# Kernel tuning notes

Measured on AMD Instinct MI355X. Metric: run time of the kernel, lower is better.

Reference implementation:

```python
import jax, jax.numpy as jnp
import numpy as np
import math

N_HEAD = 16
HEAD_DIM = 32  # n_state // n_head // 2
THETA = 10000.0
LAMBDA_INIT = 0.8 - 0.6 * math.exp(-0.3 * 12)  # depth=12
EPS = 1e-5


def _rope_tables(seq_len):
    inv = 1.0 / (THETA ** (np.arange(0, HEAD_DIM, 2, dtype=np.float32) / HEAD_DIM))  # [hd/2]
    t = np.arange(seq_len, dtype=np.float32)
    freqs = np.outer(t, inv)  # [S, hd/2]
    return jnp.asarray(np.cos(freqs)), jnp.asarray(np.sin(freqs))


def _apply_rope_interleaved(x, cos, sin):
    # x: [B,S,H,D]; cos/sin: [S,D/2]; interleaved pairs (even, odd)
    x1, x2 = x[..., 0::2], x[..., 1::2]
    c = cos[None, :, None, :]
    s = sin[None, :, None, :]
    ye = x1 * c - x2 * s
    yo = x1 * s + x2 * c
    return jnp.stack([ye, yo], axis=-1).reshape(x.shape)


def setup_inputs() -> dict:
    key = jax.random.key(0)
    ks = jax.random.split(key, 10)
    B, S, D = 1, 2048, 1024
    hd = HEAD_DIM
    inp = {
        "x": jax.random.normal(ks[0], (B, S, D), jnp.float32),
        "Wq": jax.random.normal(ks[1], (D, D), jnp.float32) * 0.02,
        "Wk": jax.random.normal(ks[2], (D, D), jnp.float32) * 0.02,
        "Wv": jax.random.normal(ks[3], (D, D), jnp.float32) * 0.02,
        "Wo": jax.random.normal(ks[4], (D, D), jnp.float32) * 0.02,
        "lambda_q1": jax.random.normal(ks[5], (hd,), jnp.float32) * 0.1,
        "lambda_k1": jax.random.normal(ks[6], (hd,), jnp.float32) * 0.1,
        "lambda_q2": jax.random.normal(ks[7], (hd,), jnp.float32) * 0.1,
        "lambda_k2": jax.random.normal(ks[8], (hd,), jnp.float32) * 0.1,
        "gamma": jnp.ones((2 * hd,), jnp.float32),
    }
    return inp


def reference(x, Wq, Wk, Wv, Wo, lambda_q1, lambda_k1, lambda_q2, lambda_k2, gamma):
    B, S, D = x.shape
    H, hd = N_HEAD, HEAD_DIM

    q = x @ Wq.T
    k = x @ Wk.T
    v = x @ Wv.T

    q = q.reshape(B, S, 2 * H, hd)
    k = k.reshape(B, S, 2 * H, hd)
    v = v.reshape(B, S, H, 2, hd)

    cos, sin = _rope_tables(S)
    q = _apply_rope_interleaved(q, cos, sin)
    k = _apply_rope_interleaved(k, cos, sin)

    q = q.reshape(B, S, H, 2, hd)
    k = k.reshape(B, S, H, 2, hd)
    q1, q2 = q[:, :, :, 0], q[:, :, :, 1]
    k1, k2 = k[:, :, :, 0], k[:, :, :, 1]
    v1, v2 = v[:, :, :, 0], v[:, :, :, 1]

    scale = hd ** -0.5
    causal = jnp.tril(jnp.ones((S, S), dtype=bool))
    neg = jnp.finfo(x.dtype).min

    def probs(qh, kh):
        s = jnp.einsum('bihd,bjhd->bhij', qh, kh) * scale
        s = jnp.where(causal[None, None], s, neg)
        return jax.nn.softmax(s, axis=-1)

    p1 = probs(q1, k1)  # reused for v1 and v2 (attn11, attn12)
    a11 = jnp.einsum('bhij,bjhd->bihd', p1, v1)
    a12 = jnp.einsum('bhij,bjhd->bihd', p1, v2)
    attn1 = jnp.concatenate([a11, a12], axis=-1)  # [B,S,H,2hd]

    p2 = probs(q2, k2)
    a21 = jnp.einsum('bhij,bjhd->bihd', p2, v1)
    a22 = jnp.einsum('bhij,bjhd->bihd', p2, v2)
    attn2 = jnp.concatenate([a21, a22], axis=-1)

    lam1 = jnp.exp(jnp.sum(lambda_q1 * lambda_k1))
    lam2 = jnp.exp(jnp.sum(lambda_q2 * lambda_k2))
    lam = lam1 - lam2 + LAMBDA_INIT

    wv = attn1 - lam * attn2
    # RMSNorm over last dim (2*hd) with affine gamma
    wv = wv * jax.lax.rsqrt(jnp.mean(wv * wv, axis=-1, keepdims=True) + EPS) * gamma
    wv = wv * (1.0 - LAMBDA_INIT)

    wv = wv.reshape(B, S, H * 2 * hd)
    return wv @ Wo.T
```

## Files before the change

### kernel.cpp

```cpp
#include <hip/hip_runtime.h>
#include <hip/hip_bf16.h>
#include <math.h>


typedef __bf16 bf16x8 __attribute__((ext_vector_type(8)));
typedef float f32x4 __attribute__((ext_vector_type(4)));
typedef float f32x16 __attribute__((ext_vector_type(16)));

#define LOG2E 1.4426950408889634f
#define SCALE 0.17677669529663687f
#define C1EXP 0.25506100319239545f
#define DMAX_THR 31.36f
#define LAM_INIT 0.783605766532f
#define ONE_M_LI 0.216394233468f

#define GLOAD16(g, l)                                                              \
  __builtin_amdgcn_global_load_lds((const __attribute__((address_space(1))) void*)(g), \
                                   (__attribute__((address_space(3))) void*)(l), 16, 0, 0)

__device__ __forceinline__ ushort f2b(float f) {
  unsigned u = __builtin_bit_cast(unsigned, f);
  u += 0x7fffu + ((u >> 16) & 1u);
  return (ushort)(u >> 16);
}
__device__ __forceinline__ float b2f(ushort h) {
  return __builtin_bit_cast(float, ((unsigned)h) << 16);
}
__device__ __forceinline__ ushort f2h(float f) {
  _Float16 h = (_Float16)f;
  return __builtin_bit_cast(ushort, h);
}
__device__ __forceinline__ float h2f(ushort u) {
  return (float)__builtin_bit_cast(_Float16, u);
}
__device__ __forceinline__ int swz128(int row, int byteoff) {
  return row * 128 + (byteoff ^ ((row & 7) << 4));
}
__device__ __forceinline__ int qoff4(int qt) {
  int G = qt >> 2, rem = qt & 3;
  return 2 * G * (G + 1) + rem * (G + 1);
}
__device__ __forceinline__ f32x16 zero16() {
  f32x16 z;
#pragma unroll
  for (int i = 0; i < 16; ++i) z[i] = 0.f;
  return z;
}

__global__ __launch_bounds__(256) void prep_kernel(
    const float* __restrict__ x, const float* __restrict__ Wq,
    const float* __restrict__ Wk, const float* __restrict__ Wv,
    const float* __restrict__ Wo,
    ushort* __restrict__ xb, ushort* __restrict__ w1, ushort* __restrict__ wob,
    float* __restrict__ cosT, float* __restrict__ sinT) {
  unsigned b = blockIdx.x;
  if (b < 3072u) {
    unsigned i8 = (b * 256u + threadIdx.x) * 8u;
    const float* s;
    ushort* d;
    if (i8 < 2097152u) { s = x + i8; d = xb + i8; }
    else if (i8 < 3145728u) { s = Wq + (i8 - 2097152u); d = w1 + (i8 - 2097152u); }
    else if (i8 < 4194304u) { s = Wk + (i8 - 3145728u); d = w1 + (i8 - 2097152u); }
    else if (i8 < 5242880u) { s = Wv + (i8 - 4194304u); d = w1 + (i8 - 2097152u); }
    else { s = Wo + (i8 - 5242880u); d = wob + (i8 - 5242880u); }
    float4 v0 = *(const float4*)s;
    float4 v1 = *(const float4*)(s + 4);
    union { ushort h[8]; uint4 u; } o;
    o.h[0] = f2b(v0.x); o.h[1] = f2b(v0.y); o.h[2] = f2b(v0.z); o.h[3] = f2b(v0.w);
    o.h[4] = f2b(v1.x); o.h[5] = f2b(v1.y); o.h[6] = f2b(v1.z); o.h[7] = f2b(v1.w);
    *(uint4*)d = o.u;
    return;
  }
  unsigned j = (b - 3072u) * 256u + threadIdx.x;
  int tt = (int)(j >> 4), jj = (int)(j & 15u);
  float inv = powf(10000.0f, -(float)(2 * jj) * (1.0f / 32.0f));
  float ang = (float)tt * inv;
  cosT[j] = cosf(ang);
  sinT[j] = sinf(ang);
}

__global__ __launch_bounds__(256) void ropetv_kernel(ushort* __restrict__ qkv,
                                                     const float* __restrict__ cosT,
                                                     const float* __restrict__ sinT,
                                                     ushort* __restrict__ vt) {
  __shared__ __align__(16) ushort tile[64][80];
  const int t = threadIdx.x;
  if (blockIdx.x < 2048u) {
    unsigned i = blockIdx.x * 256u + t;
    int row = (int)(i >> 8), u4 = (int)(i & 255u);
    int colbase = (u4 < 128) ? (u4 * 8) : (1024 + (u4 - 128) * 8);
    int pbase = u4 * 4;
    ushort* p = qkv + (size_t)row * 3072 + colbase;
    uint4 v = *(const uint4*)p;
    unsigned vv[4] = {v.x, v.y, v.z, v.w};
    unsigned ov[4];
#pragma unroll
    for (int tpp = 0; tpp < 4; ++tpp) {
      int j = (pbase + tpp) & 15;
      float c = cosT[row * 16 + j], s = sinT[row * 16 + j];
      float x1 = b2f((ushort)(vv[tpp] & 0xffffu));
      float x2 = b2f((ushort)(vv[tpp] >> 16));
      float ye = x1 * c - x2 * s;
      float yo = x1 * s + x2 * c;
      ov[tpp] = (unsigned)f2b(ye) | ((unsigned)f2b(yo) << 16);
    }
    uint4 o = {ov[0], ov[1], ov[2], ov[3]};
    *(uint4*)p = o;
    return;
  }
  const int bb = (int)blockIdx.x - 2048;
  const int d0 = (bb & 15) * 64, s0 = (bb >> 4) * 64;
#pragma unroll
  for (int p = 0; p < 2; ++p) {
    int sl = p * 32 + (t >> 3), d8 = (t & 7) * 8;
    uint4 v = *(const uint4*)(qkv + (size_t)(s0 + sl) * 3072 + 2048 + d0 + d8);
    *(uint4*)(&tile[sl][d8]) = v;
  }
  __syncthreads();
#pragma unroll
  for (int p = 0; p < 2; ++p) {
    int dl = p * 32 + (t >> 3), s8 = (t & 7) * 8;
    union { ushort h[8]; uint4 u; } tmp;
#pragma unroll
    for (int jj = 0; jj < 8; ++jj) tmp.h[jj] = tile[s8 + jj][dl];
    *(uint4*)(vt + (size_t)(d0 + dl) * 2048 + s0 + s8) = tmp.u;
  }
}

template <int BM, int BN>
__global__ __launch_bounds__(256) void gemm_bt(const ushort* __restrict__ A,
                                               const ushort* __restrict__ B,
                                               void* __restrict__ C, int M, int N, int K,
                                               int out_bf16) {
  __shared__ __align__(16) ushort As[BM * 32];
  __shared__ __align__(16) ushort Bs[BN * 32];
  const int t = threadIdx.x, lane = t & 63, w = t >> 6;
  const int g = lane >> 4, r = lane & 15;
  const int wr = w >> 1, wc = w & 1;
  const int m0 = blockIdx.y * BM, n0 = blockIdx.x * BN;
  constexpr int AM = BM / 32, AN = BN / 32;

  f32x4 acc[AM][AN];
#pragma unroll
  for (int i = 0; i < AM; ++i)
#pragma unroll
    for (int j = 0; j < AN; ++j) acc[i][j] = (f32x4){0.f, 0.f, 0.f, 0.f};

  for (int k0 = 0; k0 < K; k0 += 32) {
    __syncthreads();
#pragma unroll
    for (int p = 0; p < BM / 64; ++p) {
      int idx = p * 256 + t;
      int row = idx >> 2, ko = (idx & 3) * 8;
      GLOAD16(A + (size_t)(m0 + row) * K + k0 + ko, As + idx * 8);
    }
#pragma unroll
    for (int p = 0; p < BN / 64; ++p) {
      int idx = p * 256 + t;
      int row = idx >> 2, ko = (idx & 3) * 8;
      GLOAD16(B + (size_t)(n0 + row) * K + k0 + ko, Bs + idx * 8);
    }
    __syncthreads();
    bf16x8 af[AM], bfr[AN];
#pragma unroll
    for (int i = 0; i < AM; ++i)
      af[i] = __builtin_bit_cast(bf16x8, *(const uint4*)(As + (wr * (BM / 2) + i * 16 + r) * 32 + g * 8));
#pragma unroll
    for (int i = 0; i < AN; ++i)
      bfr[i] = __builtin_bit_cast(bf16x8, *(const uint4*)(Bs + (wc * (BN / 2) + i * 16 + r) * 32 + g * 8));
#pragma unroll
    for (int mi = 0; mi < AM; ++mi)
#pragma unroll
      for (int ni = 0; ni < AN; ++ni)
        acc[mi][ni] = __builtin_amdgcn_mfma_f32_16x16x32_bf16(af[mi], bfr[ni], acc[mi][ni], 0, 0, 0);
  }
#pragma unroll
  for (int mi = 0; mi < AM; ++mi)
#pragma unroll
    for (int ni = 0; ni < AN; ++ni)
#pragma unroll
      for (int e = 0; e < 4; ++e) {
        int row = m0 + wr * (BM / 2) + mi * 16 + g * 4 + e;
        int col = n0 + wc * (BN / 2) + ni * 16 + r;
        float v = acc[mi][ni][e];
        if (out_bf16) ((ushort*)C)[(size_t)row * N + col] = f2b(v);
        else ((float*)C)[(size_t)row * N + col] = v;
      }
}

__global__ __launch_bounds__(256, 3) void attn_split_kernel(
    const ushort* __restrict__ qkv, const ushort* __restrict__ vt,
    ushort* __restrict__ pOh, float* __restrict__ pML) {
  __shared__ __align__(16) ushort Ks[64 * 64];
  __shared__ __align__(16) ushort Vs[64 * 64];

  int wi = blockIdx.x, qt = 0, c = 0;
  for (int q = 0; q < 32; ++q) {
    int nc = (q >> 2) + 1;
    if (wi < nc) { qt = q; c = wi; break; }
    wi -= nc;
  }
  const int h = blockIdx.y;
  const int pid = h * 144 + qoff4(qt) + c;
  const int t = threadIdx.x, lane = t & 63, w = t >> 6;
  const int sub = w & 1, qh = w >> 1;
  const int ql = lane & 31, g1 = lane >> 5;
  const int qa = qt * 64 + qh * 32 + ql;

  bf16x8 qf0 = __builtin_bit_cast(bf16x8, *(const uint4*)(qkv + (size_t)qa * 3072 + h * 64 + sub * 32 + g1 * 8));
  bf16x8 qf1 = __builtin_bit_cast(bf16x8, *(const uint4*)(qkv + (size_t)qa * 3072 + h * 64 + sub * 32 + 16 + g1 * 8));

  f32x16 O0 = zero16(), O1 = zero16();
  float mm = -1e30f, lsum = 0.f;

  const int ktb = c * 4;
  const int kte = min(ktb + 4, qt + 1);
  for (int kt = ktb; kt < kte; ++kt) {
    __syncthreads();
#pragma unroll
    for (int p = 0; p < 2; ++p) {
      int idx = (p * 4 + w) * 64 + lane;
      int row = idx >> 3;
      int kbs = ((idx & 7) * 16) ^ ((row & 7) << 4);
      const ushort* gk = qkv + (size_t)(kt * 64 + row) * 3072 + 1024 + h * 64 + (kbs >> 1);
      const ushort* gv = vt + (size_t)(h * 64 + row) * 2048 + kt * 64 + (kbs >> 1);
      GLOAD16(gk, Ks + (p * 4 + w) * 512);
      GLOAD16(gv, Vs + (p * 4 + w) * 512);
    }
    __syncthreads();

    f32x16 s0 = zero16(), s1 = zero16();
    {
      const int cb0 = (sub * 32 + g1 * 8) * 2;
      bf16x8 ka = __builtin_bit_cast(bf16x8, *(const uint4*)((const char*)Ks + swz128(ql, cb0)));
      bf16x8 kb = __builtin_bit_cast(bf16x8, *(const uint4*)((const char*)Ks + swz128(32 + ql, cb0)));
      const int cb1 = (sub * 32 + 16 + g1 * 8) * 2;
      bf16x8 kc = __builtin_bit_cast(bf16x8, *(const uint4*)((const char*)Ks + swz128(ql, cb1)));
      bf16x8 kd = __builtin_bit_cast(bf16x8, *(const uint4*)((const char*)Ks + swz128(32 + ql, cb1)));
      __builtin_amdgcn_s_setprio(1);
      s0 = __builtin_amdgcn_mfma_f32_32x32x16_bf16(ka, qf0, s0, 0, 0, 0);
      s1 = __builtin_amdgcn_mfma_f32_32x32x16_bf16(kb, qf0, s1, 0, 0, 0);
      s0 = __builtin_amdgcn_mfma_f32_32x32x16_bf16(kc, qf1, s0, 0, 0, 0);
      s1 = __builtin_amdgcn_mfma_f32_32x32x16_bf16(kd, qf1, s1, 0, 0, 0);
      __builtin_amdgcn_s_setprio(0);
    }

    if (kt == qt) {
      const int lim = qh * 32 + ql;
#pragma unroll
      for (int rg = 0; rg < 16; ++rg) {
        int kv0 = (rg & 3) + 4 * g1 + 8 * (rg >> 2);
        if (kv0 > lim) s0[rg] = -1e30f;
        if (kv0 + 32 > lim) s1[rg] = -1e30f;
      }
    }

    float rm = fmaxf(s0[0], s1[0]);
#pragma unroll
    for (int rg = 1; rg < 16; ++rg) rm = fmaxf(rm, fmaxf(s0[rg], s1[rg]));
    rm = fmaxf(rm, __shfl_xor(rm, 32));

    if (!__all(rm - mm <= DMAX_THR)) {
      float mn = fmaxf(mm, rm);
      float es = exp2f((mm - mn) * C1EXP);
      mm = mn;
      lsum *= es;
      O0 *= es;
      O1 *= es;
    }
    const float mnC = mm * C1EXP;
    float ps = 0.f;
#pragma unroll
    for (int rg = 0; rg < 16; ++rg) {
      float p0 = exp2f(__builtin_fmaf(s0[rg], C1EXP, -mnC));
      float p1 = exp2f(__builtin_fmaf(s1[rg], C1EXP, -mnC));
      s0[rg] = p0; s1[rg] = p1;
      ps += p0 + p1;
    }
    ps += __shfl_xor(ps, 32);
    lsum += ps;

    unsigned pk[2][4][2];
#pragma unroll
    for (int q2 = 0; q2 < 4; ++q2) {
      float a0 = s0[4 * q2 + 0], a1 = s0[4 * q2 + 1], a2 = s0[4 * q2 + 2], a3 = s0[4 * q2 + 3];
      float b0 = s1[4 * q2 + 0], b1 = s1[4 * q2 + 1], b2 = s1[4 * q2 + 2], b3 = s1[4 * q2 + 3];
      asm("v_cvt_pk_bf16_f32 %0, %1, %2" : "=v"(pk[0][q2][0]) : "v"(a0), "v"(a1));
      asm("v_cvt_pk_bf16_f32 %0, %1, %2" : "=v"(pk[0][q2][1]) : "v"(a2), "v"(a3));
      asm("v_cvt_pk_bf16_f32 %0, %1, %2" : "=v"(pk[1][q2][0]) : "v"(b0), "v"(b1));
      asm("v_cvt_pk_bf16_f32 %0, %1, %2" : "=v"(pk[1][q2][1]) : "v"(b2), "v"(b3));
    }
#pragma unroll
    for (int kvb = 0; kvb < 2; ++kvb) {
      asm volatile("v_permlane32_swap_b32 %0, %1" : "+v"(pk[kvb][0][0]), "+v"(pk[kvb][1][0]));
      asm volatile("v_permlane32_swap_b32 %0, %1" : "+v"(pk[kvb][0][1]), "+v"(pk[kvb][1][1]));
      asm volatile("v_permlane32_swap_b32 %0, %1" : "+v"(pk[kvb][2][0]), "+v"(pk[kvb][3][0]));
      asm volatile("v_permlane32_swap_b32 %0, %1" : "+v"(pk[kvb][2][1]), "+v"(pk[kvb][3][1]));
    }

#pragma unroll
    for (int ks = 0; ks < 4; ++ks) {
      const int kvb = ks >> 1, kshi = ks & 1;
      uint4 pu;
      pu.x = pk[kvb][2 * kshi][0];
      pu.y = pk[kvb][2 * kshi][1];
      pu.z = pk[kvb][2 * kshi + 1][0];
      pu.w = pk[kvb][2 * kshi + 1][1];
      bf16x8 pf = __builtin_bit_cast(bf16x8, pu);
      const int cb = (ks * 16 + g1 * 8) * 2;
      bf16x8 v0 = __builtin_bit_cast(bf16x8, *(const uint4*)((const char*)Vs + swz128(ql, cb)));
      bf16x8 v1 = __builtin_bit_cast(bf16x8, *(const uint4*)((const char*)Vs + swz128(32 + ql, cb)));
      __builtin_amdgcn_s_setprio(1);
      O0 = __builtin_amdgcn_mfma_f32_32x32x16_bf16(v0, pf, O0, 0, 0, 0);
      O1 = __builtin_amdgcn_mfma_f32_32x32x16_bf16(v1, pf, O1, 0, 0, 0);
      __builtin_amdgcn_s_setprio(0);
    }
  }

  const int qrow = qh * 32 + ql;
  float* pml = pML + (size_t)pid * 256 + sub * 128;
  if (g1 == 0) {
    pml[qrow] = mm;
    pml[64 + qrow] = lsum;
  }
  ushort* po = pOh + ((size_t)(pid * 2 + sub) * 64 + qrow) * 64;
#pragma unroll
  for (int q2 = 0; q2 < 4; ++q2) {
    uint2 u0, u1;
    u0.x = (unsigned)f2h(O0[4 * q2 + 0]) | ((unsigned)f2h(O0[4 * q2 + 1]) << 16);
    u0.y = (unsigned)f2h(O0[4 * q2 + 2]) | ((unsigned)f2h(O0[4 * q2 + 3]) << 16);
    u1.x = (unsigned)f2h(O1[4 * q2 + 0]) | ((unsigned)f2h(O1[4 * q2 + 1]) << 16);
    u1.y = (unsigned)f2h(O1[4 * q2 + 2]) | ((unsigned)f2h(O1[4 * q2 + 3]) << 16);
    *(uint2*)(po + q2 * 8 + g1 * 4) = u0;
    *(uint2*)(po + 32 + q2 * 8 + g1 * 4) = u1;
  }
}

__global__ __launch_bounds__(256) void combine_kernel(
    const ushort* __restrict__ pOh, const float* __restrict__ pML,
    const float* __restrict__ lq1, const float* __restrict__ lk1,
    const float* __restrict__ lq2, const float* __restrict__ lk2,
    const float* __restrict__ gamma, ushort* __restrict__ attn_out) {
  const int qt = blockIdx.x, h = blockIdx.y;
  const int nc = (qt >> 2) + 1;
  const int pbase = h * 144 + qoff4(qt);
  const int t = threadIdx.x, row = t >> 2, quad = t & 3;
  const int lane = t & 63;

  float lam;
  {
    int d = lane & 31;
    float a1 = lq1[d] * lk1[d];
    float a2 = lq2[d] * lk2[d];
#pragma unroll
    for (int m = 16; m >= 1; m >>= 1) {
      a1 += __shfl_xor(a1, m);
      a2 += __shfl_xor(a2, m);
    }
    lam = expf(a1) - expf(a2) + LAM_INIT;
  }

  float M[2] = {-1e30f, -1e30f};
  for (int c = 0; c < nc; ++c) {
    const float* ml = pML + (size_t)(pbase + c) * 256;
    M[0] = fmaxf(M[0], ml[row]);
    M[1] = fmaxf(M[1], ml[128 + row]);
  }
  float L[2] = {0.f, 0.f};
  float acc[2][16];
#pragma unroll
  for (int s = 0; s < 2; ++s)
#pragma unroll
    for (int v = 0; v < 16; ++v) acc[s][v] = 0.f;

  for (int c = 0; c < nc; ++c) {
    const int pid = pbase + c;
    const float* ml = pML + (size_t)pid * 256;
#pragma unroll
    for (int s = 0; s < 2; ++s) {
      float mc = ml[s * 128 + row];
      float lc = ml[s * 128 + 64 + row];
      float wgt = exp2f((mc - M[s]) * C1EXP);
      L[s] += lc * wgt;
      const ushort* op = pOh + ((size_t)(pid * 2 + s) * 64 + row) * 64 + quad * 16;
      uint4 ua = *(const uint4*)op;
      uint4 ub = *(const uint4*)(op + 8);
      unsigned uu[8] = {ua.x, ua.y, ua.z, ua.w, ub.x, ub.y, ub.z, ub.w};
#pragma unroll
      for (int j = 0; j < 8; ++j) {
        acc[s][2 * j + 0] += h2f((ushort)(uu[j] & 0xffffu)) * wgt;
        acc[s][2 * j + 1] += h2f((ushort)(uu[j] >> 16)) * wgt;
      }
    }
  }

  float inv0 = 1.f / L[0], inv1 = 1.f / L[1];
  float wv[16], ss = 0.f;
#pragma unroll
  for (int j = 0; j < 16; ++j) {
    float val = acc[0][j] * inv0 - lam * (acc[1][j] * inv1);
    wv[j] = val;
    ss += val * val;
  }
  ss += __shfl_xor(ss, 1);
  ss += __shfl_xor(ss, 2);
  float scl = rsqrtf(ss * (1.f / 64.f) + 1e-5f) * ONE_M_LI;

  union { ushort hs[16]; uint4 u[2]; } outp;
#pragma unroll
  for (int j = 0; j < 16; ++j)
    outp.hs[j] = f2b(wv[j] * scl * gamma[quad * 16 + j]);
  uint4* dst = (uint4*)(attn_out + (size_t)(qt * 64 + row) * 1024 + h * 64 + quad * 16);
  dst[0] = outp.u[0];
  dst[1] = outp.u[1];
}

extern "C" void kernel_launch(void* const* d_in, const int* in_sizes, int n_in,
                              void* d_out, int out_size, void* d_ws, size_t ws_size,
                              hipStream_t stream) {
  const float* x = (const float*)d_in[0];
  const float* Wq = (const float*)d_in[1];
  const float* Wk = (const float*)d_in[2];
  const float* Wv = (const float*)d_in[3];
  const float* Wo = (const float*)d_in[4];
  const float* lq1 = (const float*)d_in[5];
  const float* lk1 = (const float*)d_in[6];
  const float* lq2 = (const float*)d_in[7];
  const float* lk2 = (const float*)d_in[8];
  const float* gamma = (const float*)d_in[9];
  (void)in_sizes; (void)n_in; (void)out_size; (void)ws_size;

  char* ws = (char*)d_ws;
  ushort* xb = (ushort*)(ws);
  ushort* w1 = (ushort*)(ws + (4ull << 20));
  ushort* wob = (ushort*)(ws + (10ull << 20));
  ushort* qkv = (ushort*)(ws + (12ull << 20));
  ushort* vt = (ushort*)(ws + (24ull << 20));
  ushort* atn = (ushort*)(ws + (28ull << 20));
  float* cosT = (float*)(ws + (32ull << 20));
  float* sinT = (float*)(ws + (32ull << 20) + 2048 * 16 * 4);
  const size_t pO_off = (33ull << 20);
  const size_t pml_off = pO_off + 2304ull * 2 * 64 * 64 * 2;
  ushort* pOh = (ushort*)(ws + pO_off);
  float* pML = (float*)(ws + pml_off);

  prep_kernel<<<3200, 256, 0, stream>>>(x, Wq, Wk, Wv, Wo, xb, w1, wob, cosT, sinT);
  gemm_bt<64, 128><<<dim3(24, 32), 256, 0, stream>>>(xb, w1, (void*)qkv, 2048, 3072, 1024, 1);
  ropetv_kernel<<<2560, 256, 0, stream>>>(qkv, cosT, sinT, vt);
  attn_split_kernel<<<dim3(144, 16), 256, 0, stream>>>(qkv, vt, pOh, pML);
  combine_kernel<<<dim3(32, 16), 256, 0, stream>>>(pOh, pML, lq1, lk1, lq2, lk2, gamma, atn);
  gemm_bt<64, 64><<<dim3(16, 32), 256, 0, stream>>>(atn, wob, d_out, 2048, 1024, 1024, 0);
}
```

Before: 107.7 us.

## Double K-step in GEMM with swizzled LDS and batch two attention KV tiles

The GEMM now loads a 64-wide K slice per iteration into XOR-swizzled shared memory and runs two MFMA sub-steps. This halves the number of barriers and uses a swizzle intended to avoid LDS bank conflicts. The attention split kernel now loads two K/V tiles into double-sized shared buffers behind one pair of barriers and then processes both, which reduces sync count and exposes more loads in flight. The cost is more shared memory per block, which may lower occupancy (for attention at launch bounds 3) and raise register pressure.

```diff
diff --git a/kernel.cpp b/kernel.cpp
--- a/kernel.cpp
+++ b/kernel.cpp
@@ -132,8 +132,8 @@
                                                const ushort* __restrict__ B,
                                                void* __restrict__ C, int M, int N, int K,
                                                int out_bf16) {
-  __shared__ __align__(16) ushort As[BM * 32];
-  __shared__ __align__(16) ushort Bs[BN * 32];
+  __shared__ __align__(16) ushort As[BM * 64];
+  __shared__ __align__(16) ushort Bs[BN * 64];
   const int t = threadIdx.x, lane = t & 63, w = t >> 6;
   const int g = lane >> 4, r = lane & 15;
   const int wr = w >> 1, wc = w & 1;
@@ -146,33 +146,38 @@
 #pragma unroll
     for (int j = 0; j < AN; ++j) acc[i][j] = (f32x4){0.f, 0.f, 0.f, 0.f};
 
-  for (int k0 = 0; k0 < K; k0 += 32) {
+  for (int k0 = 0; k0 < K; k0 += 64) {
     __syncthreads();
 #pragma unroll
-    for (int p = 0; p < BM / 64; ++p) {
+    for (int p = 0; p < BM / 32; ++p) {
       int idx = p * 256 + t;
-      int row = idx >> 2, ko = (idx & 3) * 8;
-      GLOAD16(A + (size_t)(m0 + row) * K + k0 + ko, As + idx * 8);
-    }
-#pragma unroll
-    for (int p = 0; p < BN / 64; ++p) {
+      int row = idx >> 3;
+      int bo = ((idx & 7) * 16) ^ ((row & 7) << 4);
+      GLOAD16(A + (size_t)(m0 + row) * K + k0 + (bo >> 1), As + idx * 8);
+    }
+#pragma unroll
+    for (int p = 0; p < BN / 32; ++p) {
       int idx = p * 256 + t;
-      int row = idx >> 2, ko = (idx & 3) * 8;
-      GLOAD16(B + (size_t)(n0 + row) * K + k0 + ko, Bs + idx * 8);
+      int row = idx >> 3;
+      int bo = ((idx & 7) * 16) ^ ((row & 7) << 4);
+      GLOAD16(B + (size_t)(n0 + row) * K + k0 + (bo >> 1), Bs + idx * 8);
     }
     __syncthreads();
-    bf16x8 af[AM], bfr[AN];
-#pragma unroll
-    for (int i = 0; i < AM; ++i)
-      af[i] = __builtin_bit_cast(bf16x8, *(const uint4*)(As + (wr * (BM / 2) + i * 16 + r) * 32 + g * 8));
-#pragma unroll
-    for (int i = 0; i < AN; ++i)
-      bfr[i] = __builtin_bit_cast(bf16x8, *(const uint4*)(Bs + (wc * (BN / 2) + i * 16 + r) * 32 + g * 8));
-#pragma unroll
-    for (int mi = 0; mi < AM; ++mi)
-#pragma unroll
-      for (int ni = 0; ni < AN; ++ni)
-        acc[mi][ni] = __builtin_amdgcn_mfma_f32_16x16x32_bf16(af[mi], bfr[ni], acc[mi][ni], 0, 0, 0);
+#pragma unroll
+    for (int ks = 0; ks < 2; ++ks) {
+      bf16x8 af[AM], bfr[AN];
+#pragma unroll
+      for (int i = 0; i < AM; ++i)
+        af[i] = __builtin_bit_cast(bf16x8, *(const uint4*)((const char*)As + swz128(wr * (BM / 2) + i * 16 + r, (ks * 32 + g * 8) * 2)));
+#pragma unroll
+      for (int i = 0; i < AN; ++i)
+        bfr[i] = __builtin_bit_cast(bf16x8, *(const uint4*)((const char*)Bs + swz128(wc * (BN / 2) + i * 16 + r, (ks * 32 + g * 8) * 2)));
+#pragma unroll
+      for (int mi = 0; mi < AM; ++mi)
+#pragma unroll
+        for (int ni = 0; ni < AN; ++ni)
+          acc[mi][ni] = __builtin_amdgcn_mfma_f32_16x16x32_bf16(af[mi], bfr[ni], acc[mi][ni], 0, 0, 0);
+    }
   }
 #pragma unroll
   for (int mi = 0; mi < AM; ++mi)
@@ -188,11 +193,24 @@
       }
 }
 
+#define ATTN_STAGE(kt_, Kb, Vb)                                                         \
+  do {                                                                                  \
+    _Pragma("unroll") for (int p_ = 0; p_ < 2; ++p_) {                                  \
+      int idx_ = (p_ * 4 + w) * 64 + lane;                                              \
+      int row_ = idx_ >> 3;                                                             \
+      int kbs_ = ((idx_ & 7) * 16) ^ ((row_ & 7) << 4);                                 \
+      const ushort* gk_ = qkv + (size_t)((kt_) * 64 + row_) * 3072 + 1024 + h * 64 + (kbs_ >> 1); \
+      const ushort* gv_ = vt + (size_t)(h * 64 + row_) * 2048 + (kt_) * 64 + (kbs_ >> 1);         \
+      GLOAD16(gk_, (Kb) + (p_ * 4 + w) * 512);                                          \
+      GLOAD16(gv_, (Vb) + (p_ * 4 + w) * 512);                                          \
+    }                                                                                   \
+  } while (0)
+
 __global__ __launch_bounds__(256, 3) void attn_split_kernel(
     const ushort* __restrict__ qkv, const ushort* __restrict__ vt,
     ushort* __restrict__ pOh, float* __restrict__ pML) {
-  __shared__ __align__(16) ushort Ks[64 * 64];
-  __shared__ __align__(16) ushort Vs[64 * 64];
+  __shared__ __align__(16) ushort Ks[2][64 * 64];
+  __shared__ __align__(16) ushort Vs[2][64 * 64];
 
   int wi = blockIdx.x, qt = 0, c = 0;
   for (int q = 0; q < 32; ++q) {
@@ -213,30 +231,18 @@
   f32x16 O0 = zero16(), O1 = zero16();
   float mm = -1e30f, lsum = 0.f;
 
-  const int ktb = c * 4;
-  const int kte = min(ktb + 4, qt + 1);
-  for (int kt = ktb; kt < kte; ++kt) {
-    __syncthreads();
-#pragma unroll
-    for (int p = 0; p < 2; ++p) {
-      int idx = (p * 4 + w) * 64 + lane;
-      int row = idx >> 3;
-      int kbs = ((idx & 7) * 16) ^ ((row & 7) << 4);
-      const ushort* gk = qkv + (size_t)(kt * 64 + row) * 3072 + 1024 + h * 64 + (kbs >> 1);
-      const ushort* gv = vt + (size_t)(h * 64 + row) * 2048 + kt * 64 + (kbs >> 1);
-      GLOAD16(gk, Ks + (p * 4 + w) * 512);
-      GLOAD16(gv, Vs + (p * 4 + w) * 512);
-    }
-    __syncthreads();
+  auto do_tile = [&](int kt, const ushort* Ksb, const ushort* Vsb) {
+    const char* Kc = (const char*)Ksb;
+    const char* Vc = (const char*)Vsb;
 
     f32x16 s0 = zero16(), s1 = zero16();
     {
       const int cb0 = (sub * 32 + g1 * 8) * 2;
-      bf16x8 ka = __builtin_bit_cast(bf16x8, *(const uint4*)((const char*)Ks + swz128(ql, cb0)));
-      bf16x8 kb = __builtin_bit_cast(bf16x8, *(const uint4*)((const char*)Ks + swz128(32 + ql, cb0)));
+      bf16x8 ka = __builtin_bit_cast(bf16x8, *(const uint4*)(Kc + swz128(ql, cb0)));
+      bf16x8 kb = __builtin_bit_cast(bf16x8, *(const uint4*)(Kc + swz128(32 + ql, cb0)));
       const int cb1 = (sub * 32 + 16 + g1 * 8) * 2;
-      bf16x8 kc = __builtin_bit_cast(bf16x8, *(const uint4*)((const char*)Ks + swz128(ql, cb1)));
-      bf16x8 kd = __builtin_bit_cast(bf16x8, *(const uint4*)((const char*)Ks + swz128(32 + ql, cb1)));
+      bf16x8 kc = __builtin_bit_cast(bf16x8, *(const uint4*)(Kc + swz128(ql, cb1)));
+      bf16x8 kd = __builtin_bit_cast(bf16x8, *(const uint4*)(Kc + swz128(32 + ql, cb1)));
       __builtin_amdgcn_s_setprio(1);
       s0 = __builtin_amdgcn_mfma_f32_32x32x16_bf16(ka, qf0, s0, 0, 0, 0);
       s1 = __builtin_amdgcn_mfma_f32_32x32x16_bf16(kb, qf0, s1, 0, 0, 0);
@@ -308,13 +314,25 @@
       pu.w = pk[kvb][2 * kshi + 1][1];
       bf16x8 pf = __builtin_bit_cast(bf16x8, pu);
       const int cb = (ks * 16 + g1 * 8) * 2;
-      bf16x8 v0 = __builtin_bit_cast(bf16x8, *(const uint4*)((const char*)Vs + swz128(ql, cb)));
-      bf16x8 v1 = __builtin_bit_cast(bf16x8, *(const uint4*)((const char*)Vs + swz128(32 + ql, cb)));
+      bf16x8 v0 = __builtin_bit_cast(bf16x8, *(const uint4*)(Vc + swz128(ql, cb)));
+      bf16x8 v1 = __builtin_bit_cast(bf16x8, *(const uint4*)(Vc + swz128(32 + ql, cb)));
       __builtin_amdgcn_s_setprio(1);
       O0 = __builtin_amdgcn_mfma_f32_32x32x16_bf16(v0, pf, O0, 0, 0, 0);
       O1 = __builtin_amdgcn_mfma_f32_32x32x16_bf16(v1, pf, O1, 0, 0, 0);
       __builtin_amdgcn_s_setprio(0);
     }
+  };
+
+  const int ktb = c * 4;
+  const int kte = min(ktb + 4, qt + 1);
+  for (int kt0 = ktb; kt0 < kte; kt0 += 2) {
+    const bool two = (kt0 + 1 < kte);
+    __syncthreads();
+    ATTN_STAGE(kt0, Ks[0], Vs[0]);
+    if (two) ATTN_STAGE(kt0 + 1, Ks[1], Vs[1]);
+    __syncthreads();
+    do_tile(kt0, Ks[0], Vs[0]);
+    if (two) do_tile(kt0 + 1, Ks[1], Vs[1]);
   }
 
   const int qrow = qh * 32 + ql;
```

Result: faster. 99.45 us (-7.7%).
